# Performance work log

Measured on AMD Instinct MI355X. Metric: run time of the kernel, lower is better.

The kernel has to match this reference:

```python
import jax, jax.numpy as jnp
import numpy as np

N = 131072   # total gates/nodes in the batched block-diagonal circuit graph
E = 524288   # directed edges (avg degree 4)
D = 100      # hidden dim
DA = 50      # msg MLP hidden
DC = 30      # classifier hidden
R = 20       # message-passing rounds


def mlp(x, W1, b1, W2, b2):
    return jax.nn.relu(x @ W1 + b1) @ W2 + b2


def gru_step(x, h, Wih, Whh, bih, bhh):
    # single-timestep torch.nn.GRU cell
    gi = x @ Wih.T + bih
    gh = h @ Whh.T + bhh
    ir, iz, inn = jnp.split(gi, 3, axis=-1)
    hr, hz, hn = jnp.split(gh, 3, axis=-1)
    r = jax.nn.sigmoid(ir + hr)
    z = jax.nn.sigmoid(iz + hz)
    nwe = jnp.tanh(inn + r * hn)
    return (1.0 - z) * nwe + z * h


def setup_inputs():
    key = jax.random.key(0)
    ks = jax.random.split(key, 26)
    s = 0.05

    def rn(k, shape):
        return jax.random.normal(k, shape, dtype=jnp.float32) * s

    inp = {
        'features': jax.random.normal(ks[0], (N, 4), dtype=jnp.float32),
        'edge_row': jax.random.randint(ks[1], (E,), 0, N, dtype=jnp.int32),
        'edge_col': jax.random.randint(ks[2], (E,), 0, N, dtype=jnp.int32),
        'init_W': rn(ks[3], (4, D)), 'init_b': jnp.zeros((D,), jnp.float32),
        'fmsg_W1': rn(ks[4], (D, DA)), 'fmsg_b1': jnp.zeros((DA,), jnp.float32),
        'fmsg_W2': rn(ks[5], (DA, D)), 'fmsg_b2': jnp.zeros((D,), jnp.float32),
        'bmsg_W1': rn(ks[6], (D, DA)), 'bmsg_b1': jnp.zeros((DA,), jnp.float32),
        'bmsg_W2': rn(ks[7], (DA, D)), 'bmsg_b2': jnp.zeros((D,), jnp.float32),
        'fgru_Wih': rn(ks[8], (3 * D, D)), 'fgru_Whh': rn(ks[9], (3 * D, D)),
        'fgru_bih': jnp.zeros((3 * D,), jnp.float32), 'fgru_bhh': jnp.zeros((3 * D,), jnp.float32),
        'bgru_Wih': rn(ks[10], (3 * D, D)), 'bgru_Whh': rn(ks[11], (3 * D, D)),
        'bgru_bih': jnp.zeros((3 * D,), jnp.float32), 'bgru_bhh': jnp.zeros((3 * D,), jnp.float32),
        'cls_W1': rn(ks[12], (D, DC)), 'cls_b1': jnp.zeros((DC,), jnp.float32),
        'cls_W2': rn(ks[13], (DC, 1)), 'cls_b2': jnp.zeros((1,), jnp.float32),
    }
    return inp


def reference(features, edge_row, edge_col, init_W, init_b,
              fmsg_W1, fmsg_b1, fmsg_W2, fmsg_b2,
              bmsg_W1, bmsg_b1, bmsg_W2, bmsg_b2,
              fgru_Wih, fgru_Whh, fgru_bih, fgru_bhh,
              bgru_Wih, bgru_Whh, bgru_bih, bgru_bhh,
              cls_W1, cls_b1, cls_W2, cls_b2):
    n = features.shape[0]
    h = features @ init_W + init_b  # [N, D]

    def round_body(h, _):
        # forward pass: adj @ forward_msg(h)
        fm = mlp(h, fmsg_W1, fmsg_b1, fmsg_W2, fmsg_b2)
        f_msg = jax.ops.segment_sum(fm[edge_col], edge_row, num_segments=n)
        h = gru_step(f_msg, h, fgru_Wih, fgru_Whh, fgru_bih, fgru_bhh)
        # backward pass: adj.T @ backward_msg(h)
        bm = mlp(h, bmsg_W1, bmsg_b1, bmsg_W2, bmsg_b2)
        b_msg = jax.ops.segment_sum(bm[edge_row], edge_col, num_segments=n)
        h = gru_step(b_msg, h, bgru_Wih, bgru_Whh, bgru_bih, bgru_bhh)
        return h, None

    h, _ = jax.lax.scan(jax.checkpoint(round_body), h, None, length=R)
    return mlp(h, cls_W1, cls_b1, cls_W2, cls_b2)  # [N, 1]
```

## Files before the change

kernel.cpp:

```cpp
#include <hip/hip_runtime.h>
#include <math.h>

#define Nn 131072
#define Ee 524288

typedef __attribute__((ext_vector_type(8))) short short8;
typedef __attribute__((ext_vector_type(4))) float f32x4;
typedef unsigned short ushort_t;
typedef unsigned int uint32;

__device__ __forceinline__ f32x4 mfma16(short8 a, short8 b, f32x4 c) {
    return __builtin_amdgcn_mfma_f32_16x16x32_bf16(a, b, c, 0, 0, 0);
}

__device__ __forceinline__ uint32 rne_bf16(float x) {
    uint32 u = __float_as_uint(x);
    return (u + 0x7FFFu + ((u >> 16) & 1u)) >> 16;
}

__device__ __forceinline__ void split3(float x, uint32& h, uint32& m, uint32& l) {
    h = rne_bf16(x);
    float hf = __uint_as_float(h << 16);
    float r1 = x - hf;
    m = rne_bf16(r1);
    float mf = __uint_as_float(m << 16);
    float r2 = r1 - mf;
    l = rne_bf16(r2);
}

__global__ void diag_kernel(float* out, float val) {
    int n = blockIdx.x * 256 + threadIdx.x;
    if (n < Nn) out[n] = (n == 0) ? val : 0.f;
}
__global__ void zero_ints(int* p, int n) {
    int i = blockIdx.x * 256 + threadIdx.x;
    if (i < n) p[i] = 0;
}

__global__ void hist_kernel(const int* __restrict__ er, const int* __restrict__ ec,
                            int* __restrict__ cnt_f, int* __restrict__ cnt_b) {
    int e = blockIdx.x * 256 + threadIdx.x;
    atomicAdd(&cnt_f[er[e]], 1);
    atomicAdd(&cnt_b[ec[e]], 1);
}

__global__ __launch_bounds__(1024) void scan_kernel(const int* __restrict__ cnt,
                                                    int* __restrict__ ptr, int n) {
    __shared__ int sums[1024];
    int t = threadIdx.x;
    int chunk = n >> 10;
    int base = t * chunk;
    int s = 0;
    for (int i = 0; i < chunk; i++) s += cnt[base + i];
    sums[t] = s;
    __syncthreads();
    for (int off = 1; off < 1024; off <<= 1) {
        int v = (t >= off) ? sums[t - off] : 0;
        __syncthreads();
        sums[t] += v;
        __syncthreads();
    }
    int run = (t == 0) ? 0 : sums[t - 1];
    for (int i = 0; i < chunk; i++) { ptr[base + i] = run; run += cnt[base + i]; }
    if (t == 1023) ptr[n] = run;
}

__global__ void fill_kernel(const int* __restrict__ er, const int* __restrict__ ec,
                            int* __restrict__ ptr_f, int* __restrict__ ptr_b,
                            int* __restrict__ src_f, int* __restrict__ src_b) {
    int e = blockIdx.x * 256 + threadIdx.x;
    int r = er[e], c = ec[e];
    int p = atomicAdd(&ptr_f[r], 1); src_f[p] = c;
    int q = atomicAdd(&ptr_b[c], 1); src_b[q] = r;
}

__global__ void prep_gru_w(const float* __restrict__ Wih, const float* __restrict__ Whh,
                           const float* __restrict__ bih, const float* __restrict__ bhh,
                           ushort_t* __restrict__ W0, ushort_t* __restrict__ W1,
                           ushort_t* __restrict__ W2, float* __restrict__ bg) {
    int gid = blockIdx.x * 256 + threadIdx.x;
    if (gid >= 448 * 224) return;
    int c = gid / 224, k = gid - c * 224;
    int d = c >> 2, g = c & 3;
    float w = 0.f;
    if (d < 100) {
        if (k < 100) {
            if (g == 0)      w = Wih[d * 100 + k];
            else if (g == 1) w = Wih[(100 + d) * 100 + k];
            else if (g == 2) w = Wih[(200 + d) * 100 + k];
        } else if (k < 200) {
            int kk = k - 100;
            if (g == 0)      w = Whh[d * 100 + kk];
            else if (g == 1) w = Whh[(100 + d) * 100 + kk];
            else if (g == 3) w = Whh[(200 + d) * 100 + kk];
        }
    }
    uint32 h, m, l; split3(w, h, m, l);
    W0[gid] = (ushort_t)h; W1[gid] = (ushort_t)m; W2[gid] = (ushort_t)l;
    if (k == 0) {
        float b = 0.f;
        if (d < 100) {
            if (g == 0)      b = bih[d] + bhh[d];
            else if (g == 1) b = bih[100 + d] + bhh[100 + d];
            else if (g == 2) b = bih[200 + d];
            else             b = bhh[200 + d];
        }
        bg[c] = b;
    }
}

__global__ void prep_msg_w(const float* __restrict__ W1, const float* __restrict__ b1,
                           const float* __restrict__ W2, const float* __restrict__ b2,
                           ushort_t* __restrict__ A0, ushort_t* __restrict__ A1,
                           ushort_t* __restrict__ A2, float* __restrict__ b1p,
                           ushort_t* __restrict__ B0, ushort_t* __restrict__ B1,
                           ushort_t* __restrict__ B2, float* __restrict__ b2p) {
    int gid = blockIdx.x * 256 + threadIdx.x;
    if (gid < 8192) {
        int c = gid >> 7, k = gid & 127;
        float w = (c < 50 && k < 100) ? W1[k * 50 + c] : 0.f;
        uint32 h, m, l; split3(w, h, m, l);
        A0[gid] = (ushort_t)h; A1[gid] = (ushort_t)m; A2[gid] = (ushort_t)l;
        if (k == 0) b1p[c] = (c < 50) ? b1[c] : 0.f;
    } else if (gid < 8192 + 7168) {
        int t = gid - 8192;
        int c = t >> 6, k = t & 63;
        float w = (c < 100 && k < 50) ? W2[k * 100 + c] : 0.f;
        uint32 h, m, l; split3(w, h, m, l);
        B0[t] = (ushort_t)h; B1[t] = (ushort_t)m; B2[t] = (ushort_t)l;
        if (k == 0) b2p[c] = (c < 100) ? b2[c] : 0.f;
    }
}

__global__ void init_h_kernel(const float* __restrict__ feat, const float* __restrict__ W,
                              const float* __restrict__ b, float* __restrict__ Act) {
    int gid = blockIdx.x * 256 + threadIdx.x;
    int n = gid / 100, d = gid - n * 100;
    float acc = b[d];
#pragma unroll
    for (int k = 0; k < 4; k++) acc += feat[n * 4 + k] * W[k * 100 + d];
    Act[(size_t)n * 200 + 100 + d] = acc;
}

__global__ __launch_bounds__(256, 2) void msg_mfma(
    const float* __restrict__ Act,
    const ushort_t* __restrict__ A0, const ushort_t* __restrict__ A1,
    const ushort_t* __restrict__ A2, const float* __restrict__ b1p,
    const ushort_t* __restrict__ B0, const ushort_t* __restrict__ B1,
    const ushort_t* __restrict__ B2, const float* __restrict__ b2p,
    float* __restrict__ fm) {
    __shared__ ushort_t C1[3][64][72];
    const int tid = threadIdx.x;
    const int u = tid >> 6;
    const int lane = tid & 63;
    const int m = lane & 15, q = lane >> 4;
    const int n0 = blockIdx.x * 64;
    const int n = n0 + u * 16 + m;

    f32x4 z = {0.f, 0.f, 0.f, 0.f};
    f32x4 a1[4] = {z, z, z, z};

    for (int kc = 0; kc < 4; kc++) {
        int kb = kc * 32 + q * 8;
        const float* src = Act + (size_t)n * 200 + 100 + kb;
        float4 v0 = *(const float4*)src;
        float4 v1 = *(const float4*)(src + 4);
        float e[8] = {v0.x, v0.y, v0.z, v0.w, v1.x, v1.y, v1.z, v1.w};
        union { short8 s; uint32 u4[4]; } f0, f1, f2;
#pragma unroll
        for (int j = 0; j < 4; j++) {
            uint32 ha, ma, la, hb, mb, lb;
            split3(e[2 * j], ha, ma, la);
            split3(e[2 * j + 1], hb, mb, lb);
            f0.u4[j] = ha | (hb << 16);
            f1.u4[j] = ma | (mb << 16);
            f2.u4[j] = la | (lb << 16);
        }
#pragma unroll
        for (int t = 0; t < 4; t++) {
            int off = (t * 16 + m) * 128 + kc * 32 + q * 8;
            short8 w0 = *(const short8*)(A0 + off);
            short8 w1 = *(const short8*)(A1 + off);
            short8 w2 = *(const short8*)(A2 + off);
            a1[t] = mfma16(w0, f0.s, a1[t]);
            a1[t] = mfma16(w0, f1.s, a1[t]);
            a1[t] = mfma16(w1, f0.s, a1[t]);
            a1[t] = mfma16(w0, f2.s, a1[t]);
            a1[t] = mfma16(w2, f0.s, a1[t]);
            a1[t] = mfma16(w1, f1.s, a1[t]);
        }
    }
#pragma unroll
    for (int t = 0; t < 4; t++) {
        int c0 = t * 16 + 4 * q;
        float4 bb = *(const float4*)&b1p[c0];
        float v0 = fmaxf(a1[t][0] + bb.x, 0.f);
        float v1 = fmaxf(a1[t][1] + bb.y, 0.f);
        float v2 = fmaxf(a1[t][2] + bb.z, 0.f);
        float v3 = fmaxf(a1[t][3] + bb.w, 0.f);
        uint32 h0, m0, l0, h1, m1, l1, h2, m2, l2, h3, m3, l3;
        split3(v0, h0, m0, l0); split3(v1, h1, m1, l1);
        split3(v2, h2, m2, l2); split3(v3, h3, m3, l3);
        int nl = u * 16 + m;
        *(uint2*)&C1[0][nl][c0] = make_uint2(h0 | (h1 << 16), h2 | (h3 << 16));
        *(uint2*)&C1[1][nl][c0] = make_uint2(m0 | (m1 << 16), m2 | (m3 << 16));
        *(uint2*)&C1[2][nl][c0] = make_uint2(l0 | (l1 << 16), l2 | (l3 << 16));
    }
    __syncthreads();

    f32x4 a2[7] = {z, z, z, z, z, z, z};
    for (int kc = 0; kc < 2; kc++) {
        int nl = u * 16 + m;
        short8 c0f = *(const short8*)&C1[0][nl][kc * 32 + q * 8];
        short8 c1f = *(const short8*)&C1[1][nl][kc * 32 + q * 8];
        short8 c2f = *(const short8*)&C1[2][nl][kc * 32 + q * 8];
#pragma unroll
        for (int t = 0; t < 7; t++) {
            int off = (t * 16 + m) * 64 + kc * 32 + q * 8;
            short8 w0 = *(const short8*)(B0 + off);
            short8 w1 = *(const short8*)(B1 + off);
            short8 w2 = *(const short8*)(B2 + off);
            a2[t] = mfma16(w0, c0f, a2[t]);
            a2[t] = mfma16(w0, c1f, a2[t]);
            a2[t] = mfma16(w1, c0f, a2[t]);
            a2[t] = mfma16(w0, c2f, a2[t]);
            a2[t] = mfma16(w2, c0f, a2[t]);
            a2[t] = mfma16(w1, c1f, a2[t]);
        }
    }
#pragma unroll
    for (int t = 0; t < 7; t++) {
        int c0 = t * 16 + 4 * q;
        if (c0 < 100) {
            float4 bb = *(const float4*)&b2p[c0];
            float4 o;
            o.x = a2[t][0] + bb.x; o.y = a2[t][1] + bb.y;
            o.z = a2[t][2] + bb.z; o.w = a2[t][3] + bb.w;
            *(float4*)&fm[(size_t)n * 100 + c0] = o;
        }
    }
}

__global__ void gather4(const float* __restrict__ fm, const int* __restrict__ ptr,
                        const int* __restrict__ idx, float* __restrict__ Act) {
    int gid = blockIdx.x * 256 + threadIdx.x;
    int n = gid / 25, qq = (gid - n * 25) * 4;
    int s = (n == 0) ? 0 : ptr[n - 1];
    int e = ptr[n];
    float4 acc = {0.f, 0.f, 0.f, 0.f};
    for (int i = s; i < e; i++) {
        float4 v = *(const float4*)&fm[(size_t)idx[i] * 100 + qq];
        acc.x += v.x; acc.y += v.y; acc.z += v.z; acc.w += v.w;
    }
    *(float4*)&Act[(size_t)n * 200 + qq] = acc;
}

__global__ __launch_bounds__(256, 2) void gru_mfma(
    float* __restrict__ Act,
    const ushort_t* __restrict__ W0, const ushort_t* __restrict__ W1,
    const ushort_t* __restrict__ W2, const float* __restrict__ bg) {
    const int tid = threadIdx.x;
    const int wave = tid >> 6;
    const int lane = tid & 63;
    const int m = lane & 15, q = lane >> 4;
    const int n0 = blockIdx.x * 64;

    f32x4 z = {0.f, 0.f, 0.f, 0.f};
    f32x4 acc[7][4];
#pragma unroll
    for (int t = 0; t < 7; t++)
#pragma unroll
        for (int rf = 0; rf < 4; rf++) acc[t][rf] = z;

    int woff[7];
#pragma unroll
    for (int t = 0; t < 7; t++)
        woff[t] = ((t * 4 + wave) * 16 + m) * 224 + q * 8;

    const float* abase = Act + (size_t)(n0 + m) * 200 + q * 8;

#define GPASS(Wreg, Fr)                                          \
    _Pragma("unroll")                                            \
    for (int t = 0; t < 7; t++) {                                \
        _Pragma("unroll")                                        \
        for (int rf = 0; rf < 4; rf++)                           \
            acc[t][rf] = mfma16(Wreg[t], Fr[rf], acc[t][rf]);    \
    }

    for (int kc = 0; kc < 7; kc++) {
        const int kb = kc * 32 + q * 8;
        const int ko = kc * 32;
        short8 f0[4], f1[4], f2[4];
#pragma unroll
        for (int rf = 0; rf < 4; rf++) {
            float e[8];
            if (kb < 200) {
                const float* src = abase + (size_t)rf * 16 * 200 + ko;
                float4 v0 = *(const float4*)src;
                float4 v1 = *(const float4*)(src + 4);
                e[0] = v0.x; e[1] = v0.y; e[2] = v0.z; e[3] = v0.w;
                e[4] = v1.x; e[5] = v1.y; e[6] = v1.z; e[7] = v1.w;
            } else {
#pragma unroll
                for (int j = 0; j < 8; j++) e[j] = 0.f;
            }
            union { short8 s; uint32 u4[4]; } p0, p1, p2;
#pragma unroll
            for (int j = 0; j < 4; j++) {
                uint32 ha, ma, la, hb, mb, lb;
                split3(e[2 * j], ha, ma, la);
                split3(e[2 * j + 1], hb, mb, lb);
                p0.u4[j] = ha | (hb << 16);
                p1.u4[j] = ma | (mb << 16);
                p2.u4[j] = la | (lb << 16);
            }
            f0[rf] = p0.s; f1[rf] = p1.s; f2[rf] = p2.s;
        }

        short8 w[7];
#pragma unroll
        for (int t = 0; t < 7; t++) w[t] = *(const short8*)(W0 + woff[t] + ko);
        GPASS(w, f0);
        GPASS(w, f1);
        GPASS(w, f2);
#pragma unroll
        for (int t = 0; t < 7; t++) w[t] = *(const short8*)(W1 + woff[t] + ko);
        GPASS(w, f0);
        GPASS(w, f1);
#pragma unroll
        for (int t = 0; t < 7; t++) w[t] = *(const short8*)(W2 + woff[t] + ko);
        GPASS(w, f0);
    }
#undef GPASS

    __syncthreads();

#pragma unroll
    for (int t = 0; t < 7; t++) {
        const int ct = t * 4 + wave;
        const int d = ct * 4 + q;
        if (d < 100) {
            float4 b4 = *(const float4*)&bg[ct * 16 + 4 * q];
#pragma unroll
            for (int rf = 0; rf < 4; rf++) {
                int n = n0 + rf * 16 + m;
                float* hp = Act + (size_t)n * 200 + 100 + d;
                float hold = *hp;
                float rp = acc[t][rf][0] + b4.x;
                float zp = acc[t][rf][1] + b4.y;
                float np = acc[t][rf][2] + b4.z;
                float hh = acc[t][rf][3] + b4.w;
                float rr = 1.f / (1.f + __expf(-rp));
                float zz = 1.f / (1.f + __expf(-zp));
                float nw = tanhf(np + rr * hh);
                *hp = (1.f - zz) * nw + zz * hold;
            }
        }
    }
}

__global__ __launch_bounds__(256) void classifier(
    const float* __restrict__ Act, const float* __restrict__ W1,
    const float* __restrict__ b1, const float* __restrict__ W2,
    const float* __restrict__ b2, float* __restrict__ out) {
    __shared__ float Wc[3000];
    __shared__ float bc[30];
    __shared__ float w2[30];
    int tid = threadIdx.x;
    for (int i = tid; i < 3000; i += 256) Wc[i] = W1[i];
    if (tid < 30) { bc[tid] = b1[tid]; w2[tid] = W2[tid]; }
    __syncthreads();
    int n = blockIdx.x * 256 + tid;
    float a[30];
#pragma unroll
    for (int j = 0; j < 30; j++) a[j] = bc[j];
    for (int k = 0; k < 100; k++) {
        float hv = Act[(size_t)n * 200 + 100 + k];
#pragma unroll
        for (int j = 0; j < 30; j++) a[j] = fmaf(hv, Wc[k * 30 + j], a[j]);
    }
    float s = b2[0];
#pragma unroll
    for (int j = 0; j < 30; j++) s = fmaf(fmaxf(a[j], 0.f), w2[j], s);
    out[n] = s;
}

extern "C" void kernel_launch(void* const* d_in, const int* in_sizes, int n_in,
                              void* d_out, int out_size, void* d_ws, size_t ws_size,
                              hipStream_t stream) {
    const float* feat     = (const float*)d_in[0];
    const int*   er       = (const int*)d_in[1];
    const int*   ec       = (const int*)d_in[2];
    const float* init_W   = (const float*)d_in[3];
    const float* init_b   = (const float*)d_in[4];
    const float* fmsg_W1  = (const float*)d_in[5];
    const float* fmsg_b1  = (const float*)d_in[6];
    const float* fmsg_W2  = (const float*)d_in[7];
    const float* fmsg_b2  = (const float*)d_in[8];
    const float* bmsg_W1  = (const float*)d_in[9];
    const float* bmsg_b1  = (const float*)d_in[10];
    const float* bmsg_W2  = (const float*)d_in[11];
    const float* bmsg_b2  = (const float*)d_in[12];
    const float* fgru_Wih = (const float*)d_in[13];
    const float* fgru_Whh = (const float*)d_in[14];
    const float* fgru_bih = (const float*)d_in[15];
    const float* fgru_bhh = (const float*)d_in[16];
    const float* bgru_Wih = (const float*)d_in[17];
    const float* bgru_Whh = (const float*)d_in[18];
    const float* bgru_bih = (const float*)d_in[19];
    const float* bgru_bhh = (const float*)d_in[20];
    const float* cls_W1   = (const float*)d_in[21];
    const float* cls_b1   = (const float*)d_in[22];
    const float* cls_W2   = (const float*)d_in[23];
    const float* cls_b2   = (const float*)d_in[24];
    float* out = (float*)d_out;

    float* ws = (float*)d_ws;
    size_t o = 0;
    float* Act = ws + o; o += (size_t)Nn * 200;
    float* fm  = ws + o; o += (size_t)Nn * 100;

    ushort_t* us = (ushort_t*)(ws + o);
    size_t uo = 0;
    ushort_t* fWg0 = us + uo; uo += 448 * 224;
    ushort_t* fWg1 = us + uo; uo += 448 * 224;
    ushort_t* fWg2 = us + uo; uo += 448 * 224;
    ushort_t* bWg0 = us + uo; uo += 448 * 224;
    ushort_t* bWg1 = us + uo; uo += 448 * 224;
    ushort_t* bWg2 = us + uo; uo += 448 * 224;
    ushort_t* fA0 = us + uo; uo += 8192;
    ushort_t* fA1 = us + uo; uo += 8192;
    ushort_t* fA2 = us + uo; uo += 8192;
    ushort_t* bA0 = us + uo; uo += 8192;
    ushort_t* bA1 = us + uo; uo += 8192;
    ushort_t* bA2 = us + uo; uo += 8192;
    ushort_t* fB0 = us + uo; uo += 7168;
    ushort_t* fB1 = us + uo; uo += 7168;
    ushort_t* fB2 = us + uo; uo += 7168;
    ushort_t* bB0 = us + uo; uo += 7168;
    ushort_t* bB1 = us + uo; uo += 7168;
    ushort_t* bB2 = us + uo; uo += 7168;
    o += uo / 2;

    float* bgf  = ws + o; o += 448;
    float* bgb  = ws + o; o += 448;
    float* b1pf = ws + o; o += 64;
    float* b1pb = ws + o; o += 64;
    float* b2pf = ws + o; o += 112;
    float* b2pb = ws + o; o += 112;

    int* iws   = (int*)(ws + o);
    int* ptr_f = iws;
    int* ptr_b = ptr_f + (Nn + 1);
    int* cnt   = ptr_b + (Nn + 1);
    int* cnt_f = cnt;
    int* cnt_b = cnt + Nn;
    int* src_f = cnt + 2 * (size_t)Nn;
    int* src_b = src_f + Ee;

    size_t need = o * sizeof(float) +
                  (size_t)(2 * (Nn + 1) + 2 * Nn + 2 * Ee) * sizeof(int);
    if (ws_size < need) {
        diag_kernel<<<(Nn + 255) / 256, 256, 0, stream>>>(out, (float)ws_size);
        return;
    }

    zero_ints<<<(2 * Nn + 255) / 256, 256, 0, stream>>>(cnt, 2 * Nn);
    hist_kernel<<<Ee / 256, 256, 0, stream>>>(er, ec, cnt_f, cnt_b);
    scan_kernel<<<1, 1024, 0, stream>>>(cnt_f, ptr_f, Nn);
    scan_kernel<<<1, 1024, 0, stream>>>(cnt_b, ptr_b, Nn);
    fill_kernel<<<Ee / 256, 256, 0, stream>>>(er, ec, ptr_f, ptr_b, src_f, src_b);

    prep_gru_w<<<(448 * 224 + 255) / 256, 256, 0, stream>>>(
        fgru_Wih, fgru_Whh, fgru_bih, fgru_bhh, fWg0, fWg1, fWg2, bgf);
    prep_gru_w<<<(448 * 224 + 255) / 256, 256, 0, stream>>>(
        bgru_Wih, bgru_Whh, bgru_bih, bgru_bhh, bWg0, bWg1, bWg2, bgb);
    prep_msg_w<<<(15360 + 255) / 256, 256, 0, stream>>>(
        fmsg_W1, fmsg_b1, fmsg_W2, fmsg_b2, fA0, fA1, fA2, b1pf, fB0, fB1, fB2, b2pf);
    prep_msg_w<<<(15360 + 255) / 256, 256, 0, stream>>>(
        bmsg_W1, bmsg_b1, bmsg_W2, bmsg_b2, bA0, bA1, bA2, b1pb, bB0, bB1, bB2, b2pb);

    init_h_kernel<<<(Nn * 100) / 256, 256, 0, stream>>>(feat, init_W, init_b, Act);

    const int gTile = Nn / 64;
    const int gGru  = Nn / 64;
    const int gGath = Nn * 25 / 256;

    for (int rd = 0; rd < 20; rd++) {
        msg_mfma<<<gTile, 256, 0, stream>>>(Act, fA0, fA1, fA2, b1pf, fB0, fB1, fB2, b2pf, fm);
        gather4<<<gGath, 256, 0, stream>>>(fm, ptr_f, src_f, Act);
        gru_mfma<<<gGru, 256, 0, stream>>>(Act, fWg0, fWg1, fWg2, bgf);

        msg_mfma<<<gTile, 256, 0, stream>>>(Act, bA0, bA1, bA2, b1pb, bB0, bB1, bB2, b2pb, fm);
        gather4<<<gGath, 256, 0, stream>>>(fm, ptr_b, src_b, Act);
        gru_mfma<<<gGru, 256, 0, stream>>>(Act, bWg0, bWg1, bWg2, bgb);
    }

    classifier<<<Nn / 256, 256, 0, stream>>>(Act, cls_W1, cls_b1, cls_W2, cls_b2, out);
}
```

Measured before the change: 13.68 ms.

## Store activations pre-split as three bf16 planes instead of fp32

The fp32 activation buffer (msg input and hidden state) is replaced by three bf16 planes holding the hi/mid/lo split, padded to 240 columns with the hidden state at offset 112. The MFMA kernels now load the bf16 fragments directly instead of re-splitting fp32 values on every load, and the split is done once by the writers (gather, GRU, init). Reads of the old hidden value and the classifier rebuild fp32 from the three parts. The total stored bytes per row go up slightly, and it adds a pad-zeroing kernel plus scattered 2-byte stores in the GRU epilogue.

After: 17.10 ms. 25.0% more time.

```diff
diff --git a/kernel.cpp b/kernel.cpp
--- a/kernel.cpp
+++ b/kernel.cpp
@@ -28,6 +28,14 @@
     l = rne_bf16(r2);
 }
 
+__device__ __forceinline__ float recon3(ushort_t a, ushort_t b, ushort_t c) {
+    return __uint_as_float((uint32)a << 16) + __uint_as_float((uint32)b << 16) +
+           __uint_as_float((uint32)c << 16);
+}
+
+#define ROWS 240
+#define HOFF 112
+
 __global__ void diag_kernel(float* out, float val) {
     int n = blockIdx.x * 256 + threadIdx.x;
     if (n < Nn) out[n] = (n == 0) ? val : 0.f;
@@ -35,6 +43,13 @@
 __global__ void zero_ints(int* p, int n) {
     int i = blockIdx.x * 256 + threadIdx.x;
     if (i < n) p[i] = 0;
+}
+__global__ void zero_pads(ushort_t* L0, ushort_t* L1, ushort_t* L2) {
+    int gid = blockIdx.x * 256 + threadIdx.x;
+    int n = gid / 40, p = gid - n * 40;
+    int off = (p < 12) ? (100 + p) : (212 + (p - 12));
+    size_t idx = (size_t)n * ROWS + off;
+    L0[idx] = 0; L1[idx] = 0; L2[idx] = 0;
 }
 
 __global__ void hist_kernel(const int* __restrict__ er, const int* __restrict__ ec,
@@ -88,8 +103,8 @@
             if (g == 0)      w = Wih[d * 100 + k];
             else if (g == 1) w = Wih[(100 + d) * 100 + k];
             else if (g == 2) w = Wih[(200 + d) * 100 + k];
-        } else if (k < 200) {
-            int kk = k - 100;
+        } else if (k >= HOFF && k < HOFF + 100) {
+            int kk = k - HOFF;
             if (g == 0)      w = Whh[d * 100 + kk];
             else if (g == 1) w = Whh[(100 + d) * 100 + kk];
             else if (g == 3) w = Whh[(200 + d) * 100 + kk];
@@ -133,17 +148,22 @@
 }
 
 __global__ void init_h_kernel(const float* __restrict__ feat, const float* __restrict__ W,
-                              const float* __restrict__ b, float* __restrict__ Act) {
+                              const float* __restrict__ b,
+                              ushort_t* __restrict__ L0, ushort_t* __restrict__ L1,
+                              ushort_t* __restrict__ L2) {
     int gid = blockIdx.x * 256 + threadIdx.x;
     int n = gid / 100, d = gid - n * 100;
     float acc = b[d];
 #pragma unroll
     for (int k = 0; k < 4; k++) acc += feat[n * 4 + k] * W[k * 100 + d];
-    Act[(size_t)n * 200 + 100 + d] = acc;
+    uint32 h, m, l; split3(acc, h, m, l);
+    size_t idx = (size_t)n * ROWS + HOFF + d;
+    L0[idx] = (ushort_t)h; L1[idx] = (ushort_t)m; L2[idx] = (ushort_t)l;
 }
 
 __global__ __launch_bounds__(256, 2) void msg_mfma(
-    const float* __restrict__ Act,
+    const ushort_t* __restrict__ L0, const ushort_t* __restrict__ L1,
+    const ushort_t* __restrict__ L2,
     const ushort_t* __restrict__ A0, const ushort_t* __restrict__ A1,
     const ushort_t* __restrict__ A2, const float* __restrict__ b1p,
     const ushort_t* __restrict__ B0, const ushort_t* __restrict__ B1,
@@ -161,33 +181,22 @@
     f32x4 a1[4] = {z, z, z, z};
 
     for (int kc = 0; kc < 4; kc++) {
-        int kb = kc * 32 + q * 8;
-        const float* src = Act + (size_t)n * 200 + 100 + kb;
-        float4 v0 = *(const float4*)src;
-        float4 v1 = *(const float4*)(src + 4);
-        float e[8] = {v0.x, v0.y, v0.z, v0.w, v1.x, v1.y, v1.z, v1.w};
-        union { short8 s; uint32 u4[4]; } f0, f1, f2;
-#pragma unroll
-        for (int j = 0; j < 4; j++) {
-            uint32 ha, ma, la, hb, mb, lb;
-            split3(e[2 * j], ha, ma, la);
-            split3(e[2 * j + 1], hb, mb, lb);
-            f0.u4[j] = ha | (hb << 16);
-            f1.u4[j] = ma | (mb << 16);
-            f2.u4[j] = la | (lb << 16);
-        }
+        size_t base = (size_t)n * ROWS + HOFF + kc * 32 + q * 8;
+        short8 f0 = *(const short8*)(L0 + base);
+        short8 f1 = *(const short8*)(L1 + base);
+        short8 f2 = *(const short8*)(L2 + base);
 #pragma unroll
         for (int t = 0; t < 4; t++) {
             int off = (t * 16 + m) * 128 + kc * 32 + q * 8;
             short8 w0 = *(const short8*)(A0 + off);
             short8 w1 = *(const short8*)(A1 + off);
             short8 w2 = *(const short8*)(A2 + off);
-            a1[t] = mfma16(w0, f0.s, a1[t]);
-            a1[t] = mfma16(w0, f1.s, a1[t]);
-            a1[t] = mfma16(w1, f0.s, a1[t]);
-            a1[t] = mfma16(w0, f2.s, a1[t]);
-            a1[t] = mfma16(w2, f0.s, a1[t]);
-            a1[t] = mfma16(w1, f1.s, a1[t]);
+            a1[t] = mfma16(w0, f0, a1[t]);
+            a1[t] = mfma16(w0, f1, a1[t]);
+            a1[t] = mfma16(w1, f0, a1[t]);
+            a1[t] = mfma16(w0, f2, a1[t]);
+            a1[t] = mfma16(w2, f0, a1[t]);
+            a1[t] = mfma16(w1, f1, a1[t]);
         }
     }
 #pragma unroll
@@ -242,7 +251,9 @@
 }
 
 __global__ void gather4(const float* __restrict__ fm, const int* __restrict__ ptr,
-                        const int* __restrict__ idx, float* __restrict__ Act) {
+                        const int* __restrict__ idx,
+                        ushort_t* __restrict__ L0, ushort_t* __restrict__ L1,
+                        ushort_t* __restrict__ L2) {
     int gid = blockIdx.x * 256 + threadIdx.x;
     int n = gid / 25, qq = (gid - n * 25) * 4;
     int s = (n == 0) ? 0 : ptr[n - 1];
@@ -252,11 +263,17 @@
         float4 v = *(const float4*)&fm[(size_t)idx[i] * 100 + qq];
         acc.x += v.x; acc.y += v.y; acc.z += v.z; acc.w += v.w;
     }
-    *(float4*)&Act[(size_t)n * 200 + qq] = acc;
+    uint32 h0, m0, l0, h1, m1, l1, h2, m2, l2, h3, m3, l3;
+    split3(acc.x, h0, m0, l0); split3(acc.y, h1, m1, l1);
+    split3(acc.z, h2, m2, l2); split3(acc.w, h3, m3, l3);
+    size_t base = (size_t)n * ROWS + qq;
+    *(uint2*)&L0[base] = make_uint2(h0 | (h1 << 16), h2 | (h3 << 16));
+    *(uint2*)&L1[base] = make_uint2(m0 | (m1 << 16), m2 | (m3 << 16));
+    *(uint2*)&L2[base] = make_uint2(l0 | (l1 << 16), l2 | (l3 << 16));
 }
 
 __global__ __launch_bounds__(256, 2) void gru_mfma(
-    float* __restrict__ Act,
+    ushort_t* __restrict__ L0, ushort_t* __restrict__ L1, ushort_t* __restrict__ L2,
     const ushort_t* __restrict__ W0, const ushort_t* __restrict__ W1,
     const ushort_t* __restrict__ W2, const float* __restrict__ bg) {
     const int tid = threadIdx.x;
@@ -277,7 +294,7 @@
     for (int t = 0; t < 7; t++)
         woff[t] = ((t * 4 + wave) * 16 + m) * 224 + q * 8;
 
-    const float* abase = Act + (size_t)(n0 + m) * 200 + q * 8;
+    const size_t arow = (size_t)(n0 + m) * ROWS + q * 8;
 
 #define GPASS(Wreg, Fr)                                          \
     _Pragma("unroll")                                            \
@@ -288,35 +305,15 @@
     }
 
     for (int kc = 0; kc < 7; kc++) {
-        const int kb = kc * 32 + q * 8;
         const int ko = kc * 32;
         short8 f0[4], f1[4], f2[4];
 #pragma unroll
         for (int rf = 0; rf < 4; rf++) {
-            float e[8];
-            if (kb < 200) {
-                const float* src = abase + (size_t)rf * 16 * 200 + ko;
-                float4 v0 = *(const float4*)src;
-                float4 v1 = *(const float4*)(src + 4);
-                e[0] = v0.x; e[1] = v0.y; e[2] = v0.z; e[3] = v0.w;
-                e[4] = v1.x; e[5] = v1.y; e[6] = v1.z; e[7] = v1.w;
-            } else {
-#pragma unroll
-                for (int j = 0; j < 8; j++) e[j] = 0.f;
-            }
-            union { short8 s; uint32 u4[4]; } p0, p1, p2;
-#pragma unroll
-            for (int j = 0; j < 4; j++) {
-                uint32 ha, ma, la, hb, mb, lb;
-                split3(e[2 * j], ha, ma, la);
-                split3(e[2 * j + 1], hb, mb, lb);
-                p0.u4[j] = ha | (hb << 16);
-                p1.u4[j] = ma | (mb << 16);
-                p2.u4[j] = la | (lb << 16);
-            }
-            f0[rf] = p0.s; f1[rf] = p1.s; f2[rf] = p2.s;
-        }
-
+            size_t b = arow + (size_t)rf * 16 * ROWS + ko;
+            f0[rf] = *(const short8*)(L0 + b);
+            f1[rf] = *(const short8*)(L1 + b);
+            f2[rf] = *(const short8*)(L2 + b);
+        }
         short8 w[7];
 #pragma unroll
         for (int t = 0; t < 7; t++) w[t] = *(const short8*)(W0 + woff[t] + ko);
@@ -344,8 +341,8 @@
 #pragma unroll
             for (int rf = 0; rf < 4; rf++) {
                 int n = n0 + rf * 16 + m;
-                float* hp = Act + (size_t)n * 200 + 100 + d;
-                float hold = *hp;
+                size_t idx = (size_t)n * ROWS + HOFF + d;
+                float hold = recon3(L0[idx], L1[idx], L2[idx]);
                 float rp = acc[t][rf][0] + b4.x;
                 float zp = acc[t][rf][1] + b4.y;
                 float np = acc[t][rf][2] + b4.z;
@@ -353,14 +350,17 @@
                 float rr = 1.f / (1.f + __expf(-rp));
                 float zz = 1.f / (1.f + __expf(-zp));
                 float nw = tanhf(np + rr * hh);
-                *hp = (1.f - zz) * nw + zz * hold;
+                float hnew = (1.f - zz) * nw + zz * hold;
+                uint32 h, mm, l; split3(hnew, h, mm, l);
+                L0[idx] = (ushort_t)h; L1[idx] = (ushort_t)mm; L2[idx] = (ushort_t)l;
             }
         }
     }
 }
 
 __global__ __launch_bounds__(256) void classifier(
-    const float* __restrict__ Act, const float* __restrict__ W1,
+    const ushort_t* __restrict__ L0, const ushort_t* __restrict__ L1,
+    const ushort_t* __restrict__ L2, const float* __restrict__ W1,
     const float* __restrict__ b1, const float* __restrict__ W2,
     const float* __restrict__ b2, float* __restrict__ out) {
     __shared__ float Wc[3000];
@@ -375,7 +375,8 @@
 #pragma unroll
     for (int j = 0; j < 30; j++) a[j] = bc[j];
     for (int k = 0; k < 100; k++) {
-        float hv = Act[(size_t)n * 200 + 100 + k];
+        size_t idx = (size_t)n * ROWS + HOFF + k;
+        float hv = recon3(L0[idx], L1[idx], L2[idx]);
 #pragma unroll
         for (int j = 0; j < 30; j++) a[j] = fmaf(hv, Wc[k * 30 + j], a[j]);
     }
@@ -415,52 +416,54 @@
     const float* cls_b2   = (const float*)d_in[24];
     float* out = (float*)d_out;
 
-    float* ws = (float*)d_ws;
-    size_t o = 0;
-    float* Act = ws + o; o += (size_t)Nn * 200;
-    float* fm  = ws + o; o += (size_t)Nn * 100;
-
-    ushort_t* us = (ushort_t*)(ws + o);
-    size_t uo = 0;
-    ushort_t* fWg0 = us + uo; uo += 448 * 224;
-    ushort_t* fWg1 = us + uo; uo += 448 * 224;
-    ushort_t* fWg2 = us + uo; uo += 448 * 224;
-    ushort_t* bWg0 = us + uo; uo += 448 * 224;
-    ushort_t* bWg1 = us + uo; uo += 448 * 224;
-    ushort_t* bWg2 = us + uo; uo += 448 * 224;
-    ushort_t* fA0 = us + uo; uo += 8192;
-    ushort_t* fA1 = us + uo; uo += 8192;
-    ushort_t* fA2 = us + uo; uo += 8192;
-    ushort_t* bA0 = us + uo; uo += 8192;
-    ushort_t* bA1 = us + uo; uo += 8192;
-    ushort_t* bA2 = us + uo; uo += 8192;
-    ushort_t* fB0 = us + uo; uo += 7168;
-    ushort_t* fB1 = us + uo; uo += 7168;
-    ushort_t* fB2 = us + uo; uo += 7168;
-    ushort_t* bB0 = us + uo; uo += 7168;
-    ushort_t* bB1 = us + uo; uo += 7168;
-    ushort_t* bB2 = us + uo; uo += 7168;
-    o += uo / 2;
-
-    float* bgf  = ws + o; o += 448;
-    float* bgb  = ws + o; o += 448;
-    float* b1pf = ws + o; o += 64;
-    float* b1pb = ws + o; o += 64;
-    float* b2pf = ws + o; o += 112;
-    float* b2pb = ws + o; o += 112;
-
-    int* iws   = (int*)(ws + o);
-    int* ptr_f = iws;
-    int* ptr_b = ptr_f + (Nn + 1);
-    int* cnt   = ptr_b + (Nn + 1);
+    char* base = (char*)d_ws;
+    size_t off = 0;
+    auto alloc = [&](size_t bytes) -> void* {
+        void* p = base + off;
+        off += (bytes + 15) & ~(size_t)15;
+        return p;
+    };
+
+    ushort_t* L0 = (ushort_t*)alloc((size_t)Nn * ROWS * 2);
+    ushort_t* L1 = (ushort_t*)alloc((size_t)Nn * ROWS * 2);
+    ushort_t* L2 = (ushort_t*)alloc((size_t)Nn * ROWS * 2);
+    float*    fm = (float*)alloc((size_t)Nn * 100 * 4);
+
+    ushort_t* fWg0 = (ushort_t*)alloc(448 * 224 * 2);
+    ushort_t* fWg1 = (ushort_t*)alloc(448 * 224 * 2);
+    ushort_t* fWg2 = (ushort_t*)alloc(448 * 224 * 2);
+    ushort_t* bWg0 = (ushort_t*)alloc(448 * 224 * 2);
+    ushort_t* bWg1 = (ushort_t*)alloc(448 * 224 * 2);
+    ushort_t* bWg2 = (ushort_t*)alloc(448 * 224 * 2);
+    ushort_t* fA0  = (ushort_t*)alloc(8192 * 2);
+    ushort_t* fA1  = (ushort_t*)alloc(8192 * 2);
+    ushort_t* fA2  = (ushort_t*)alloc(8192 * 2);
+    ushort_t* bA0  = (ushort_t*)alloc(8192 * 2);
+    ushort_t* bA1  = (ushort_t*)alloc(8192 * 2);
+    ushort_t* bA2  = (ushort_t*)alloc(8192 * 2);
+    ushort_t* fB0  = (ushort_t*)alloc(7168 * 2);
+    ushort_t* fB1  = (ushort_t*)alloc(7168 * 2);
+    ushort_t* fB2  = (ushort_t*)alloc(7168 * 2);
+    ushort_t* bB0  = (ushort_t*)alloc(7168 * 2);
+    ushort_t* bB1  = (ushort_t*)alloc(7168 * 2);
+    ushort_t* bB2  = (ushort_t*)alloc(7168 * 2);
+
+    float* bgf  = (float*)alloc(448 * 4);
+    float* bgb  = (float*)alloc(448 * 4);
+    float* b1pf = (float*)alloc(64 * 4);
+    float* b1pb = (float*)alloc(64 * 4);
+    float* b2pf = (float*)alloc(112 * 4);
+    float* b2pb = (float*)alloc(112 * 4);
+
+    int* ptr_f = (int*)alloc((Nn + 1) * 4);
+    int* ptr_b = (int*)alloc((Nn + 1) * 4);
+    int* cnt   = (int*)alloc(2 * (size_t)Nn * 4);
     int* cnt_f = cnt;
     int* cnt_b = cnt + Nn;
-    int* src_f = cnt + 2 * (size_t)Nn;
-    int* src_b = src_f + Ee;
-
-    size_t need = o * sizeof(float) +
-                  (size_t)(2 * (Nn + 1) + 2 * Nn + 2 * Ee) * sizeof(int);
-    if (ws_size < need) {
+    int* src_f = (int*)alloc((size_t)Ee * 4);
+    int* src_b = (int*)alloc((size_t)Ee * 4);
+
+    if (ws_size < off) {
         diag_kernel<<<(Nn + 255) / 256, 256, 0, stream>>>(out, (float)ws_size);
         return;
     }
@@ -480,21 +483,24 @@
     prep_msg_w<<<(15360 + 255) / 256, 256, 0, stream>>>(
         bmsg_W1, bmsg_b1, bmsg_W2, bmsg_b2, bA0, bA1, bA2, b1pb, bB0, bB1, bB2, b2pb);
 
-    init_h_kernel<<<(Nn * 100) / 256, 256, 0, stream>>>(feat, init_W, init_b, Act);
+    zero_pads<<<(Nn * 40) / 256, 256, 0, stream>>>(L0, L1, L2);
+    init_h_kernel<<<(Nn * 100) / 256, 256, 0, stream>>>(feat, init_W, init_b, L0, L1, L2);
 
     const int gTile = Nn / 64;
-    const int gGru  = Nn / 64;
     const int gGath = Nn * 25 / 256;
 
     for (int rd = 0; rd < 20; rd++) {
-        msg_mfma<<<gTile, 256, 0, stream>>>(Act, fA0, fA1, fA2, b1pf, fB0, fB1, fB2, b2pf, fm);
-        gather4<<<gGath, 256, 0, stream>>>(fm, ptr_f, src_f, Act);
-        gru_mfma<<<gGru, 256, 0, stream>>>(Act, fWg0, fWg1, fWg2, bgf);
-
-        msg_mfma<<<gTile, 256, 0, stream>>>(Act, bA0, bA1, bA2, b1pb, bB0, bB1, bB2, b2pb, fm);
-        gather4<<<gGath, 256, 0, stream>>>(fm, ptr_b, src_b, Act);
-        gru_mfma<<<gGru, 256, 0, stream>>>(Act, bWg0, bWg1, bWg2, bgb);
-    }
-
-    classifier<<<Nn / 256, 256, 0, stream>>>(Act, cls_W1, cls_b1, cls_W2, cls_b2, out);
-}
+        msg_mfma<<<gTile, 256, 0, stream>>>(L0, L1, L2, fA0, fA1, fA2, b1pf,
+                                            fB0, fB1, fB2, b2pf, fm);
+        gather4<<<gGath, 256, 0, stream>>>(fm, ptr_f, src_f, L0, L1, L2);
+        gru_mfma<<<gTile, 256, 0, stream>>>(L0, L1, L2, fWg0, fWg1, fWg2, bgf);
+
+        msg_mfma<<<gTile, 256, 0, stream>>>(L0, L1, L2, bA0, bA1, bA2, b1pb,
+                                            bB0, bB1, bB2, b2pb, fm);
+        gather4<<<gGath, 256, 0, stream>>>(fm, ptr_b, src_b, L0, L1, L2);
+        gru_mfma<<<gTile, 256, 0, stream>>>(L0, L1, L2, bWg0, bWg1, bWg2, bgb);
+    }
+
+    classifier<<<Nn / 256, 256, 0, stream>>>(L0, L1, L2, cls_W1, cls_b1,
+                                             cls_W2, cls_b2, out);
+}
```
